# Optimization experiments

Hardware: AMD Instinct MI355X
Metric: run time of the kernel (lower is better)

Reference implementation:

```python
import jax, jax.numpy as jnp
import numpy as np

B, NH, NKV, HD, SW, D = 32, 32, 8, 128, 4096, 4096
G = NH // NKV  # GQA group size


def setup_inputs() -> dict:
    key = jax.random.key(0)
    ks = jax.random.split(key, 7)
    x = jax.random.normal(ks[0], (1, 1, B, D), jnp.float32)
    wqkv = jax.random.normal(ks[1], (D, NH * HD + 2 * NKV * HD), jnp.float32) * 0.02
    wo = jax.random.normal(ks[2], (D, D), jnp.float32) * 0.02
    rot_mat = jax.random.normal(ks[3], (HD, HD), jnp.float32) * 0.1
    cache_k = jax.random.normal(ks[4], (B, NKV, SW, HD), jnp.float32)
    cache_v = jax.random.normal(ks[5], (B, NKV, SW, HD), jnp.float32)
    attn_mask = jnp.zeros((1, NH, B, SW), jnp.float32)
    return {"x": x, "wqkv": wqkv, "wo": wo, "rot_mat": rot_mat,
            "cache_k": cache_k, "cache_v": cache_v,
            "attn_mask": attn_mask, "current_pos": 4095}


def reference(x, wqkv, wo, rot_mat, cache_k, cache_v, attn_mask, current_pos):
    # start_pos advanced to 4096 -> padded_layer_past_len = layer_slice = SW (full window)
    scale = jnp.asarray(HD, x.dtype) ** -0.5
    # fused QKV projection: (B, D) @ (D, 6144)
    xqkv = x[0, 0] @ wqkv  # (B, NH*HD + 2*NKV*HD)
    q = xqkv[:, : NH * HD].reshape(B, NH, HD)
    k = xqkv[:, NH * HD: NH * HD + NKV * HD].reshape(B, NKV, HD)
    v = xqkv[:, NH * HD + NKV * HD:].reshape(B, NKV, HD)
    # matrix-form rotary embedding for the current position
    q = q @ rot_mat  # (B, NH, HD)
    k = k @ rot_mat  # (B, NKV, HD)
    # KV-cache update at current_pos
    keys = cache_k.at[:, :, current_pos, :].set(k)    # (B, NKV, SW, HD)
    values = cache_v.at[:, :, current_pos, :].set(v)  # (B, NKV, SW, HD)
    # GQA sliding-window attention over the (full) window
    qg = (q * scale).reshape(B, NKV, G, HD)
    scores = jnp.einsum('bkgd,bksd->bkgs', qg, keys)  # (B, NKV, G, SW)
    mask = jnp.transpose(attn_mask[0], (1, 0, 2)).reshape(B, NKV, G, SW)
    probs = jax.nn.softmax(scores + mask, axis=-1)
    ctx = jnp.einsum('bkgs,bksd->bkgd', probs, values)  # (B, NKV, G, HD)
    # concatenate heads + output projection
    out = ctx.reshape(B, NH * HD) @ wo  # (B, D)
    return out.reshape(1, 1, B, D)
```

## Files before the change

### kernel.cpp

```cpp
#include <hip/hip_runtime.h>

#define BB 32
#define NHH 32
#define NKVV 8
#define HDD 128
#define SWW 4096
#define DD 4096
#define GG 4
#define QKVC 6144
#define NSPLIT 16
#define CHUNK (SWW / NSPLIT)
#define KSPB 16

__global__ __launch_bounds__(256) void skinny_gemm_part(
    const float* __restrict__ x, const float* __restrict__ w,
    float* __restrict__ part, int K, int ncols) {
  __shared__ float2 red[4][64][8];
  const int t = threadIdx.x;
  const int ct = t & 63, kg = t >> 6;
  const long c0 = (long)blockIdx.x * 128 + ct * 2;
  const int Kb = K / KSPB;
  const int klen = Kb / 4;
  const int k0 = blockIdx.y * Kb + kg * klen;
  float2 acc[BB];
#pragma unroll
  for (int r = 0; r < BB; ++r) acc[r] = make_float2(0.f, 0.f);

#pragma unroll 2
  for (int k = k0; k < k0 + klen; k += 4) {
    float2 wv0 = *(const float2*)&w[(long)(k + 0) * ncols + c0];
    float2 wv1 = *(const float2*)&w[(long)(k + 1) * ncols + c0];
    float2 wv2 = *(const float2*)&w[(long)(k + 2) * ncols + c0];
    float2 wv3 = *(const float2*)&w[(long)(k + 3) * ncols + c0];
#pragma unroll
    for (int r = 0; r < BB; ++r) {
      float4 xv = *(const float4*)&x[r * K + k];
      acc[r].x = fmaf(xv.x, wv0.x, acc[r].x);
      acc[r].y = fmaf(xv.x, wv0.y, acc[r].y);
      acc[r].x = fmaf(xv.y, wv1.x, acc[r].x);
      acc[r].y = fmaf(xv.y, wv1.y, acc[r].y);
      acc[r].x = fmaf(xv.z, wv2.x, acc[r].x);
      acc[r].y = fmaf(xv.z, wv2.y, acc[r].y);
      acc[r].x = fmaf(xv.w, wv3.x, acc[r].x);
      acc[r].y = fmaf(xv.w, wv3.y, acc[r].y);
    }
  }
  for (int rc = 0; rc < 4; ++rc) {
    if (rc) __syncthreads();
#pragma unroll
    for (int j = 0; j < 8; ++j) red[kg][ct][j] = acc[rc * 8 + j];
    __syncthreads();
    if (kg == 0) {
#pragma unroll
      for (int j = 0; j < 8; ++j) {
        float2 s0 = red[0][ct][j], s1 = red[1][ct][j];
        float2 s2 = red[2][ct][j], s3 = red[3][ct][j];
        float2 sm = make_float2((s0.x + s1.x) + (s2.x + s3.x),
                                (s0.y + s1.y) + (s2.y + s3.y));
        *(float2*)&part[((long)blockIdx.y * BB + rc * 8 + j) * ncols + c0] = sm;
      }
    }
  }
}

__global__ __launch_bounds__(256) void reduce_part(
    const float* __restrict__ part, float* __restrict__ out, long n) {
  long i = (long)blockIdx.x * 256 + threadIdx.x;
  if (i >= n) return;
  float s = 0.f;
#pragma unroll
  for (int j = 0; j < KSPB; ++j) s += part[(long)j * n + i];
  out[i] = s;
}

__global__ __launch_bounds__(128) void rotary_kernel(
    const float* __restrict__ xqkv, const float* __restrict__ rot,
    float* __restrict__ q_rot, float* __restrict__ k_rot) {
  __shared__ float vec[HDD];
  const int blk = blockIdx.x;
  const int j = threadIdx.x;
  const float* src;
  float* dst;
  if (blk < BB * NHH) {
    int b = blk >> 5, h = blk & 31;
    src = xqkv + (long)b * QKVC + h * HDD;
    dst = q_rot + (long)(b * NHH + h) * HDD;
  } else {
    int i = blk - BB * NHH;
    int b = i >> 3, kv = i & 7;
    src = xqkv + (long)b * QKVC + NHH * HDD + kv * HDD;
    dst = k_rot + (long)(b * NKVV + kv) * HDD;
  }
  vec[j] = src[j];
  __syncthreads();
  float a0 = 0.f, a1 = 0.f, a2 = 0.f, a3 = 0.f;
#pragma unroll
  for (int d0 = 0; d0 < HDD; d0 += 4) {
    a0 += vec[d0 + 0] * rot[(d0 + 0) * HDD + j];
    a1 += vec[d0 + 1] * rot[(d0 + 1) * HDD + j];
    a2 += vec[d0 + 2] * rot[(d0 + 2) * HDD + j];
    a3 += vec[d0 + 3] * rot[(d0 + 3) * HDD + j];
  }
  dst[j] = (a0 + a1) + (a2 + a3);
}

__global__ __launch_bounds__(256) void attn_partial(
    const float* __restrict__ q_rot, const float* __restrict__ k_rot,
    const float* __restrict__ xqkv, const float* __restrict__ cache_k,
    const float* __restrict__ cache_v, const float* __restrict__ mask,
    const int* __restrict__ curpos, float* __restrict__ pm,
    float* __restrict__ pl, float* __restrict__ pacc) {
  __shared__ float4 scp[CHUNK];
  __shared__ float4 mkp[CHUNK];
  __shared__ float red[4][GG][HDD];

  const int blk = blockIdx.x;
  const int split = blk & (NSPLIT - 1);
  const int bkv = blk >> 4;
  const int b = bkv >> 3, kv = bkv & 7;
  const int cur = curpos[0];
  const int s0 = split * CHUNK;
  const int t = threadIdx.x, lane = t & 63, w = t >> 6;
  const int lg = lane & 15;
  const float scale = 0.08838834764831845f;

  for (int i = t; i < GG * CHUNK; i += 256) {
    int g = i >> 8;
    int sl = i & (CHUNK - 1);
    ((float*)mkp)[sl * 4 + g] =
        mask[((long)(kv * GG + g) * BB + b) * SWW + s0 + sl];
  }

  float4 qa[GG], qb[GG];
#pragma unroll
  for (int g = 0; g < GG; ++g) {
    const float4* qp =
        (const float4*)(q_rot + (long)((b * NHH + kv * GG + g) * HDD));
    qa[g] = qp[lg];
    qb[g] = qp[lg + 16];
  }
  const float* kbase = cache_k + (long)(b * NKVV + kv) * SWW * HDD;
  const float* knew = k_rot + (long)(b * NKVV + kv) * HDD;
  __syncthreads();

#pragma unroll 2
  for (int it = 0; it < CHUNK / 16; ++it) {
    int sloc = it * 16 + w * 4 + (lane >> 4);
    int s = s0 + sloc;
    const float4* kp =
        (const float4*)((s == cur) ? knew : (kbase + (long)s * HDD));
    float4 ka = kp[lg];
    float4 kb = kp[lg + 16];
    float dots[GG];
#pragma unroll
    for (int g = 0; g < GG; ++g) {
      dots[g] = ka.x * qa[g].x + ka.y * qa[g].y + ka.z * qa[g].z +
                ka.w * qa[g].w + kb.x * qb[g].x + kb.y * qb[g].y +
                kb.z * qb[g].z + kb.w * qb[g].w;
    }
#pragma unroll
    for (int m = 1; m < 16; m <<= 1) {
#pragma unroll
      for (int g = 0; g < GG; ++g) dots[g] += __shfl_xor(dots[g], m);
    }
    if (lg == 0) {
      float4 mv = mkp[sloc];
      float4 sv;
      sv.x = fmaf(dots[0], scale, mv.x);
      sv.y = fmaf(dots[1], scale, mv.y);
      sv.z = fmaf(dots[2], scale, mv.z);
      sv.w = fmaf(dots[3], scale, mv.w);
      scp[sloc] = sv;
    }
  }
  __syncthreads();

  const int sl = w * 64 + lane;
  float4 e = scp[sl];
  float4 mx = e;
#pragma unroll
  for (int m = 1; m < 64; m <<= 1) {
    mx.x = fmaxf(mx.x, __shfl_xor(mx.x, m));
    mx.y = fmaxf(mx.y, __shfl_xor(mx.y, m));
    mx.z = fmaxf(mx.z, __shfl_xor(mx.z, m));
    mx.w = fmaxf(mx.w, __shfl_xor(mx.w, m));
  }
  if (lane == 0) *(float4*)&red[w][0][0] = mx;
  __syncthreads();
  float4 m0 = *(const float4*)&red[0][0][0];
  float4 m1 = *(const float4*)&red[1][0][0];
  float4 m2 = *(const float4*)&red[2][0][0];
  float4 m3 = *(const float4*)&red[3][0][0];
  float4 Mx;
  Mx.x = fmaxf(fmaxf(m0.x, m1.x), fmaxf(m2.x, m3.x));
  Mx.y = fmaxf(fmaxf(m0.y, m1.y), fmaxf(m2.y, m3.y));
  Mx.z = fmaxf(fmaxf(m0.z, m1.z), fmaxf(m2.z, m3.z));
  Mx.w = fmaxf(fmaxf(m0.w, m1.w), fmaxf(m2.w, m3.w));
  float4 p;
  p.x = __expf(e.x - Mx.x);
  p.y = __expf(e.y - Mx.y);
  p.z = __expf(e.z - Mx.z);
  p.w = __expf(e.w - Mx.w);
  scp[sl] = p;
  float4 sm = p;
#pragma unroll
  for (int m = 1; m < 64; m <<= 1) {
    sm.x += __shfl_xor(sm.x, m);
    sm.y += __shfl_xor(sm.y, m);
    sm.z += __shfl_xor(sm.z, m);
    sm.w += __shfl_xor(sm.w, m);
  }
  if (lane == 0) *(float4*)&red[w][1][0] = sm;
  __syncthreads();
  float4 t0 = *(const float4*)&red[0][1][0];
  float4 t1 = *(const float4*)&red[1][1][0];
  float4 t2 = *(const float4*)&red[2][1][0];
  float4 t3 = *(const float4*)&red[3][1][0];
  if (t == 0) {
    long base = ((long)(b * NHH + kv * GG)) * NSPLIT + split;
    pm[base + 0 * NSPLIT] = Mx.x;
    pm[base + 1 * NSPLIT] = Mx.y;
    pm[base + 2 * NSPLIT] = Mx.z;
    pm[base + 3 * NSPLIT] = Mx.w;
    pl[base + 0 * NSPLIT] = (t0.x + t1.x) + (t2.x + t3.x);
    pl[base + 1 * NSPLIT] = (t0.y + t1.y) + (t2.y + t3.y);
    pl[base + 2 * NSPLIT] = (t0.z + t1.z) + (t2.z + t3.z);
    pl[base + 3 * NSPLIT] = (t0.w + t1.w) + (t2.w + t3.w);
  }
  __syncthreads();

  const float* vbase = cache_v + (long)(b * NKVV + kv) * SWW * HDD;
  const float* vnew =
      xqkv + (long)b * QKVC + NHH * HDD + NKVV * HDD + kv * HDD;
  const int dl = lane & 31;
  const int half = lane >> 5;
  float4 acc0 = make_float4(0, 0, 0, 0), acc1 = acc0, acc2 = acc0,
         acc3 = acc0;
#pragma unroll 4
  for (int it = 0; it < 32; ++it) {
    int slp = w * 64 + it * 2 + half;
    float4 v4 = *(const float4*)(vbase + (long)(s0 + slp) * HDD + dl * 4);
    float4 p4 = scp[slp];
    acc0.x = fmaf(p4.x, v4.x, acc0.x);
    acc0.y = fmaf(p4.x, v4.y, acc0.y);
    acc0.z = fmaf(p4.x, v4.z, acc0.z);
    acc0.w = fmaf(p4.x, v4.w, acc0.w);
    acc1.x = fmaf(p4.y, v4.x, acc1.x);
    acc1.y = fmaf(p4.y, v4.y, acc1.y);
    acc1.z = fmaf(p4.y, v4.z, acc1.z);
    acc1.w = fmaf(p4.y, v4.w, acc1.w);
    acc2.x = fmaf(p4.z, v4.x, acc2.x);
    acc2.y = fmaf(p4.z, v4.y, acc2.y);
    acc2.z = fmaf(p4.z, v4.z, acc2.z);
    acc2.w = fmaf(p4.z, v4.w, acc2.w);
    acc3.x = fmaf(p4.w, v4.x, acc3.x);
    acc3.y = fmaf(p4.w, v4.y, acc3.y);
    acc3.z = fmaf(p4.w, v4.z, acc3.z);
    acc3.w = fmaf(p4.w, v4.w, acc3.w);
  }
  if (cur >= s0 && cur < s0 + CHUNK) {
    int slc = cur - s0;
    if (w == (slc >> 6) && half == (slc & 1)) {
      float4 p4 = scp[slc];
      float4 vc = *(const float4*)(vbase + (long)cur * HDD + dl * 4);
      float4 vn = *(const float4*)(vnew + dl * 4);
      float4 d;
      d.x = vn.x - vc.x;
      d.y = vn.y - vc.y;
      d.z = vn.z - vc.z;
      d.w = vn.w - vc.w;
      acc0.x = fmaf(p4.x, d.x, acc0.x);
      acc0.y = fmaf(p4.x, d.y, acc0.y);
      acc0.z = fmaf(p4.x, d.z, acc0.z);
      acc0.w = fmaf(p4.x, d.w, acc0.w);
      acc1.x = fmaf(p4.y, d.x, acc1.x);
      acc1.y = fmaf(p4.y, d.y, acc1.y);
      acc1.z = fmaf(p4.y, d.z, acc1.z);
      acc1.w = fmaf(p4.y, d.w, acc1.w);
      acc2.x = fmaf(p4.z, d.x, acc2.x);
      acc2.y = fmaf(p4.z, d.y, acc2.y);
      acc2.z = fmaf(p4.z, d.z, acc2.z);
      acc2.w = fmaf(p4.z, d.w, acc2.w);
      acc3.x = fmaf(p4.w, d.x, acc3.x);
      acc3.y = fmaf(p4.w, d.y, acc3.y);
      acc3.z = fmaf(p4.w, d.z, acc3.z);
      acc3.w = fmaf(p4.w, d.w, acc3.w);
    }
  }
  acc0.x += __shfl_xor(acc0.x, 32);
  acc0.y += __shfl_xor(acc0.y, 32);
  acc0.z += __shfl_xor(acc0.z, 32);
  acc0.w += __shfl_xor(acc0.w, 32);
  acc1.x += __shfl_xor(acc1.x, 32);
  acc1.y += __shfl_xor(acc1.y, 32);
  acc1.z += __shfl_xor(acc1.z, 32);
  acc1.w += __shfl_xor(acc1.w, 32);
  acc2.x += __shfl_xor(acc2.x, 32);
  acc2.y += __shfl_xor(acc2.y, 32);
  acc2.z += __shfl_xor(acc2.z, 32);
  acc2.w += __shfl_xor(acc2.w, 32);
  acc3.x += __shfl_xor(acc3.x, 32);
  acc3.y += __shfl_xor(acc3.y, 32);
  acc3.z += __shfl_xor(acc3.z, 32);
  acc3.w += __shfl_xor(acc3.w, 32);
  if (half == 0) {
    *(float4*)&red[w][0][dl * 4] = acc0;
    *(float4*)&red[w][1][dl * 4] = acc1;
    *(float4*)&red[w][2][dl * 4] = acc2;
    *(float4*)&red[w][3][dl * 4] = acc3;
  }
  __syncthreads();
  if (t < HDD) {
#pragma unroll
    for (int g = 0; g < GG; ++g) {
      float s = (red[0][g][t] + red[1][g][t]) + (red[2][g][t] + red[3][g][t]);
      pacc[(((long)(b * NHH + kv * GG + g)) * NSPLIT + split) * HDD + t] = s;
    }
  }
}

__global__ __launch_bounds__(128) void attn_combine(
    const float* __restrict__ pm, const float* __restrict__ pl,
    const float* __restrict__ pacc, float* __restrict__ ctx) {
  const int bh = blockIdx.x;
  const int d = threadIdx.x;
  float M = -1e30f;
#pragma unroll
  for (int i = 0; i < NSPLIT; ++i) M = fmaxf(M, pm[bh * NSPLIT + i]);
  float L = 0.f, a = 0.f;
#pragma unroll
  for (int i = 0; i < NSPLIT; ++i) {
    float wexp = __expf(pm[bh * NSPLIT + i] - M);
    L += pl[bh * NSPLIT + i] * wexp;
    a += wexp * pacc[((long)bh * NSPLIT + i) * HDD + d];
  }
  ctx[(long)bh * HDD + d] = a / L;
}

extern "C" void kernel_launch(void* const* d_in, const int* in_sizes, int n_in,
                              void* d_out, int out_size, void* d_ws,
                              size_t ws_size, hipStream_t stream) {
  const float* x = (const float*)d_in[0];
  const float* wqkv = (const float*)d_in[1];
  const float* wo = (const float*)d_in[2];
  const float* rot = (const float*)d_in[3];
  const float* cache_k = (const float*)d_in[4];
  const float* cache_v = (const float*)d_in[5];
  const float* mask = (const float*)d_in[6];
  const int* curpos = (const int*)d_in[7];
  float* out = (float*)d_out;

  float* ws = (float*)d_ws;
  float* xqkv = ws;
  float* q_rot = xqkv + 196608;
  float* k_rot = q_rot + 131072;
  float* pm = k_rot + 32768;
  float* pl = pm + 16384;
  float* ctx = pl + 16384;
  float* big = ctx + 131072;
  (void)in_sizes; (void)n_in; (void)out_size; (void)ws_size;

  hipLaunchKernelGGL(skinny_gemm_part, dim3(QKVC / 128, KSPB), dim3(256), 0,
                     stream, x, wqkv, big, DD, QKVC);
  hipLaunchKernelGGL(reduce_part, dim3((BB * QKVC) / 256), dim3(256), 0,
                     stream, big, xqkv, (long)BB * QKVC);
  hipLaunchKernelGGL(rotary_kernel, dim3(BB * NHH + BB * NKVV), dim3(128), 0,
                     stream, xqkv, rot, q_rot, k_rot);
  hipLaunchKernelGGL(attn_partial, dim3(BB * NKVV * NSPLIT), dim3(256), 0,
                     stream, q_rot, k_rot, xqkv, cache_k, cache_v, mask,
                     curpos, pm, pl, big);
  hipLaunchKernelGGL(attn_combine, dim3(BB * NHH), dim3(128), 0, stream, pm,
                     pl, big, ctx);
  hipLaunchKernelGGL(skinny_gemm_part, dim3(DD / 128, KSPB), dim3(256), 0,
                     stream, ctx, wo, big, DD, DD);
  hipLaunchKernelGGL(reduce_part, dim3((BB * DD) / 256), dim3(256), 0, stream,
                     big, out, (long)BB * DD);
}
```

Before: 385.8 us.

## Make each attention wavefront an independent split to remove block barriers

The number of block splits is halved, and each of the four wavefronts now processes its own 128-key slice with private score and mask buffers. Each wavefront emits its own partial max, sum and accumulator, so there are 32 partials per head. This removes every __syncthreads and the cross-wave shared-memory reduction inside attn_partial. The cost is more partial data written to global memory and a longer combine loop, and the grid shrinks to 2048 blocks.

```diff
diff --git a/kernel.cpp b/kernel.cpp
--- a/kernel.cpp
+++ b/kernel.cpp
@@ -8,8 +8,10 @@
 #define DD 4096
 #define GG 4
 #define QKVC 6144
-#define NSPLIT 16
+#define NSPLIT 8
 #define CHUNK (SWW / NSPLIT)
+#define WKEYS 128
+#define NS2 (NSPLIT * 4)
 #define KSPB 16
 
 __global__ __launch_bounds__(256) void skinny_gemm_part(
@@ -110,25 +112,25 @@
     const float* __restrict__ cache_v, const float* __restrict__ mask,
     const int* __restrict__ curpos, float* __restrict__ pm,
     float* __restrict__ pl, float* __restrict__ pacc) {
-  __shared__ float4 scp[CHUNK];
-  __shared__ float4 mkp[CHUNK];
-  __shared__ float red[4][GG][HDD];
+  __shared__ float4 scp[4][WKEYS];
+  __shared__ float4 mkp[4][WKEYS];
 
   const int blk = blockIdx.x;
   const int split = blk & (NSPLIT - 1);
-  const int bkv = blk >> 4;
+  const int bkv = blk >> 3;
   const int b = bkv >> 3, kv = bkv & 7;
   const int cur = curpos[0];
-  const int s0 = split * CHUNK;
   const int t = threadIdx.x, lane = t & 63, w = t >> 6;
+  const int sw0 = split * CHUNK + w * WKEYS;
   const int lg = lane & 15;
+  const int grp = lane >> 4;
   const float scale = 0.08838834764831845f;
 
-  for (int i = t; i < GG * CHUNK; i += 256) {
-    int g = i >> 8;
-    int sl = i & (CHUNK - 1);
-    ((float*)mkp)[sl * 4 + g] =
-        mask[((long)(kv * GG + g) * BB + b) * SWW + s0 + sl];
+  for (int i = lane; i < GG * WKEYS; i += 64) {
+    int g = i >> 7;
+    int sl = i & (WKEYS - 1);
+    ((float*)&mkp[w][0])[sl * 4 + g] =
+        mask[((long)(kv * GG + g) * BB + b) * SWW + sw0 + sl];
   }
 
   float4 qa[GG], qb[GG];
@@ -141,12 +143,11 @@
   }
   const float* kbase = cache_k + (long)(b * NKVV + kv) * SWW * HDD;
   const float* knew = k_rot + (long)(b * NKVV + kv) * HDD;
-  __syncthreads();
 
 #pragma unroll 2
-  for (int it = 0; it < CHUNK / 16; ++it) {
-    int sloc = it * 16 + w * 4 + (lane >> 4);
-    int s = s0 + sloc;
+  for (int it = 0; it < WKEYS / 4; ++it) {
+    int sloc = it * 4 + grp;
+    int s = sw0 + sloc;
     const float4* kp =
         (const float4*)((s == cur) ? knew : (kbase + (long)s * HDD));
     float4 ka = kp[lg];
@@ -164,20 +165,23 @@
       for (int g = 0; g < GG; ++g) dots[g] += __shfl_xor(dots[g], m);
     }
     if (lg == 0) {
-      float4 mv = mkp[sloc];
+      float4 mv = mkp[w][sloc];
       float4 sv;
       sv.x = fmaf(dots[0], scale, mv.x);
       sv.y = fmaf(dots[1], scale, mv.y);
       sv.z = fmaf(dots[2], scale, mv.z);
       sv.w = fmaf(dots[3], scale, mv.w);
-      scp[sloc] = sv;
-    }
-  }
-  __syncthreads();
-
-  const int sl = w * 64 + lane;
-  float4 e = scp[sl];
-  float4 mx = e;
+      scp[w][sloc] = sv;
+    }
+  }
+
+  float4 e0 = scp[w][lane];
+  float4 e1 = scp[w][lane + 64];
+  float4 mx;
+  mx.x = fmaxf(e0.x, e1.x);
+  mx.y = fmaxf(e0.y, e1.y);
+  mx.z = fmaxf(e0.z, e1.z);
+  mx.w = fmaxf(e0.w, e1.w);
 #pragma unroll
   for (int m = 1; m < 64; m <<= 1) {
     mx.x = fmaxf(mx.x, __shfl_xor(mx.x, m));
@@ -185,24 +189,22 @@
     mx.z = fmaxf(mx.z, __shfl_xor(mx.z, m));
     mx.w = fmaxf(mx.w, __shfl_xor(mx.w, m));
   }
-  if (lane == 0) *(float4*)&red[w][0][0] = mx;
-  __syncthreads();
-  float4 m0 = *(const float4*)&red[0][0][0];
-  float4 m1 = *(const float4*)&red[1][0][0];
-  float4 m2 = *(const float4*)&red[2][0][0];
-  float4 m3 = *(const float4*)&red[3][0][0];
-  float4 Mx;
-  Mx.x = fmaxf(fmaxf(m0.x, m1.x), fmaxf(m2.x, m3.x));
-  Mx.y = fmaxf(fmaxf(m0.y, m1.y), fmaxf(m2.y, m3.y));
-  Mx.z = fmaxf(fmaxf(m0.z, m1.z), fmaxf(m2.z, m3.z));
-  Mx.w = fmaxf(fmaxf(m0.w, m1.w), fmaxf(m2.w, m3.w));
-  float4 p;
-  p.x = __expf(e.x - Mx.x);
-  p.y = __expf(e.y - Mx.y);
-  p.z = __expf(e.z - Mx.z);
-  p.w = __expf(e.w - Mx.w);
-  scp[sl] = p;
-  float4 sm = p;
+  float4 p0, p1;
+  p0.x = __expf(e0.x - mx.x);
+  p0.y = __expf(e0.y - mx.y);
+  p0.z = __expf(e0.z - mx.z);
+  p0.w = __expf(e0.w - mx.w);
+  p1.x = __expf(e1.x - mx.x);
+  p1.y = __expf(e1.y - mx.y);
+  p1.z = __expf(e1.z - mx.z);
+  p1.w = __expf(e1.w - mx.w);
+  scp[w][lane] = p0;
+  scp[w][lane + 64] = p1;
+  float4 sm;
+  sm.x = p0.x + p1.x;
+  sm.y = p0.y + p1.y;
+  sm.z = p0.z + p1.z;
+  sm.w = p0.w + p1.w;
 #pragma unroll
   for (int m = 1; m < 64; m <<= 1) {
     sm.x += __shfl_xor(sm.x, m);
@@ -210,24 +212,18 @@
     sm.z += __shfl_xor(sm.z, m);
     sm.w += __shfl_xor(sm.w, m);
   }
-  if (lane == 0) *(float4*)&red[w][1][0] = sm;
-  __syncthreads();
-  float4 t0 = *(const float4*)&red[0][1][0];
-  float4 t1 = *(const float4*)&red[1][1][0];
-  float4 t2 = *(const float4*)&red[2][1][0];
-  float4 t3 = *(const float4*)&red[3][1][0];
-  if (t == 0) {
-    long base = ((long)(b * NHH + kv * GG)) * NSPLIT + split;
-    pm[base + 0 * NSPLIT] = Mx.x;
-    pm[base + 1 * NSPLIT] = Mx.y;
-    pm[base + 2 * NSPLIT] = Mx.z;
-    pm[base + 3 * NSPLIT] = Mx.w;
-    pl[base + 0 * NSPLIT] = (t0.x + t1.x) + (t2.x + t3.x);
-    pl[base + 1 * NSPLIT] = (t0.y + t1.y) + (t2.y + t3.y);
-    pl[base + 2 * NSPLIT] = (t0.z + t1.z) + (t2.z + t3.z);
-    pl[base + 3 * NSPLIT] = (t0.w + t1.w) + (t2.w + t3.w);
-  }
-  __syncthreads();
+  const int sp = split * 4 + w;
+  if (lane == 0) {
+    long base = ((long)(b * NHH + kv * GG)) * NS2 + sp;
+    pm[base + 0 * NS2] = mx.x;
+    pm[base + 1 * NS2] = mx.y;
+    pm[base + 2 * NS2] = mx.z;
+    pm[base + 3 * NS2] = mx.w;
+    pl[base + 0 * NS2] = sm.x;
+    pl[base + 1 * NS2] = sm.y;
+    pl[base + 2 * NS2] = sm.z;
+    pl[base + 3 * NS2] = sm.w;
+  }
 
   const float* vbase = cache_v + (long)(b * NKVV + kv) * SWW * HDD;
   const float* vnew =
@@ -237,10 +233,10 @@
   float4 acc0 = make_float4(0, 0, 0, 0), acc1 = acc0, acc2 = acc0,
          acc3 = acc0;
 #pragma unroll 4
-  for (int it = 0; it < 32; ++it) {
-    int slp = w * 64 + it * 2 + half;
-    float4 v4 = *(const float4*)(vbase + (long)(s0 + slp) * HDD + dl * 4);
-    float4 p4 = scp[slp];
+  for (int it = 0; it < WKEYS / 2; ++it) {
+    int slp = it * 2 + half;
+    float4 v4 = *(const float4*)(vbase + (long)(sw0 + slp) * HDD + dl * 4);
+    float4 p4 = scp[w][slp];
     acc0.x = fmaf(p4.x, v4.x, acc0.x);
     acc0.y = fmaf(p4.x, v4.y, acc0.y);
     acc0.z = fmaf(p4.x, v4.z, acc0.z);
@@ -258,10 +254,10 @@
     acc3.z = fmaf(p4.w, v4.z, acc3.z);
     acc3.w = fmaf(p4.w, v4.w, acc3.w);
   }
-  if (cur >= s0 && cur < s0 + CHUNK) {
-    int slc = cur - s0;
-    if (w == (slc >> 6) && half == (slc & 1)) {
-      float4 p4 = scp[slc];
+  {
+    int slc = cur - sw0;
+    if (slc >= 0 && slc < WKEYS && half == (slc & 1)) {
+      float4 p4 = scp[w][slc];
       float4 vc = *(const float4*)(vbase + (long)cur * HDD + dl * 4);
       float4 vn = *(const float4*)(vnew + dl * 4);
       float4 d;
@@ -304,18 +300,11 @@
   acc3.z += __shfl_xor(acc3.z, 32);
   acc3.w += __shfl_xor(acc3.w, 32);
   if (half == 0) {
-    *(float4*)&red[w][0][dl * 4] = acc0;
-    *(float4*)&red[w][1][dl * 4] = acc1;
-    *(float4*)&red[w][2][dl * 4] = acc2;
-    *(float4*)&red[w][3][dl * 4] = acc3;
-  }
-  __syncthreads();
-  if (t < HDD) {
-#pragma unroll
-    for (int g = 0; g < GG; ++g) {
-      float s = (red[0][g][t] + red[1][g][t]) + (red[2][g][t] + red[3][g][t]);
-      pacc[(((long)(b * NHH + kv * GG + g)) * NSPLIT + split) * HDD + t] = s;
-    }
+    const long hb = (long)(b * NHH + kv * GG);
+    *(float4*)&pacc[((hb + 0) * NS2 + sp) * HDD + dl * 4] = acc0;
+    *(float4*)&pacc[((hb + 1) * NS2 + sp) * HDD + dl * 4] = acc1;
+    *(float4*)&pacc[((hb + 2) * NS2 + sp) * HDD + dl * 4] = acc2;
+    *(float4*)&pacc[((hb + 3) * NS2 + sp) * HDD + dl * 4] = acc3;
   }
 }
 
@@ -326,13 +315,13 @@
   const int d = threadIdx.x;
   float M = -1e30f;
 #pragma unroll
-  for (int i = 0; i < NSPLIT; ++i) M = fmaxf(M, pm[bh * NSPLIT + i]);
+  for (int i = 0; i < NS2; ++i) M = fmaxf(M, pm[bh * NS2 + i]);
   float L = 0.f, a = 0.f;
-#pragma unroll
-  for (int i = 0; i < NSPLIT; ++i) {
-    float wexp = __expf(pm[bh * NSPLIT + i] - M);
-    L += pl[bh * NSPLIT + i] * wexp;
-    a += wexp * pacc[((long)bh * NSPLIT + i) * HDD + d];
+#pragma unroll 8
+  for (int i = 0; i < NS2; ++i) {
+    float wexp = __expf(pm[bh * NS2 + i] - M);
+    L += pl[bh * NS2 + i] * wexp;
+    a += wexp * pacc[((long)bh * NS2 + i) * HDD + d];
   }
   ctx[(long)bh * HDD + d] = a / L;
 }
@@ -355,8 +344,8 @@
   float* q_rot = xqkv + 196608;
   float* k_rot = q_rot + 131072;
   float* pm = k_rot + 32768;
-  float* pl = pm + 16384;
-  float* ctx = pl + 16384;
+  float* pl = pm + 32768;
+  float* ctx = pl + 32768;
   float* big = ctx + 131072;
   (void)in_sizes; (void)n_in; (void)out_size; (void)ws_size;
 
```

Result: slower. 407.4 us (+5.6%).
